# Kernel tuning notes

Hardware: AMD Instinct MI355X
Metric: run time of the kernel (lower is better)

Reference implementation:

```python
import jax, jax.numpy as jnp
import numpy as np

TMSG = 15  # max_len - 1


def setup_inputs() -> dict:
    key = jax.random.key(0)
    ks = jax.random.split(key, 8)
    B, T_in, E, H, V = 4096, 4, 256, 512, 32000
    s = lambda k, shape: jax.random.normal(k, shape, jnp.float32) * 0.05
    return {
        "inp": jax.random.normal(ks[0], (B, T_in, E), jnp.float32),
        "Wx0": s(ks[1], (E, 4 * H)),
        "Wh0": s(ks[2], (H, 4 * H)),
        "b0": jnp.zeros((4 * H,), jnp.float32),
        "Wx1": s(ks[3], (H, 4 * H)),
        "Wh1": s(ks[4], (H, 4 * H)),
        "b1": jnp.zeros((4 * H,), jnp.float32),
        "Wd": s(ks[5], (H, V)),
        "bd": jnp.zeros((V,), jnp.float32),
    }


def _lstm_step(x, h, c, Wx, Wh, b):
    # Keras LSTMCell gate order: i, f, g(cell), o
    z = x @ Wx + h @ Wh + b
    i, f, g, o = jnp.split(z, 4, axis=-1)
    c = jax.nn.sigmoid(f) * c + jax.nn.sigmoid(i) * jnp.tanh(g)
    h = jax.nn.sigmoid(o) * jnp.tanh(c)
    return h, c


def reference(inp, Wx0, Wh0, b0, Wx1, Wh1, b1, Wd, bd):
    B = inp.shape[0]
    H = Wh0.shape[0]
    z = jnp.zeros((B, H), inp.dtype)

    def scan_fn(carry, x_t):
        h0, c0, h1, c1 = carry
        h0, c0 = _lstm_step(x_t, h0, c0, Wx0, Wh0, b0)
        h1, c1 = _lstm_step(h0, h1, c1, Wx1, Wh1, b1)
        return (h0, c0, h1, c1), None

    # NOTE: source bug resets initial_state to None every step, so each of the
    # max_len-1 steps runs the identical stacked LSTM from zero state; we run it once.
    (h0, c0, h1, c1), _ = jax.lax.scan(scan_fn, (z, z, z, z), jnp.swapaxes(inp, 0, 1))
    out = h1  # (B, H) last-step output of top cell

    log_probs = jax.nn.log_softmax(out @ Wd + bd, axis=-1)  # (B, V)
    probs = jnp.exp(log_probs)
    entropy = -jnp.sum(probs * log_probs, axis=-1)  # (B,)

    keys = jax.random.split(jax.random.key(42), TMSG)
    samples = jax.vmap(lambda k: jax.random.categorical(k, log_probs, axis=-1))(keys)  # (T, B)
    lp = log_probs[jnp.arange(B)[None, :], samples]  # (T, B) log_prob of sampled chars
    ent = jnp.broadcast_to(entropy[None], (TMSG, B))  # (T, B)

    message = samples.T  # (B, T)
    message = jnp.concatenate([message, jnp.zeros_like(message)], axis=1)  # (B, 2T)
    state_h = jnp.stack([h0, c0])  # keras unpack quirk: states[0] = [h, c] of cell 0
    return (message, lp, ent, state_h)
```

## Files before the change

### kernel.cpp

```cpp
#include <hip/hip_runtime.h>
#include <stdint.h>
#include <math.h>

#define BB 4096
#define HH 512
#define VV 32000
#define NT 15
#define STF 2097152

struct KeysArg { uint32_t w[2*NT]; };

__host__ __device__ inline void tf2x32(uint32_t k0, uint32_t k1,
                                       uint32_t x0, uint32_t x1,
                                       uint32_t& o0, uint32_t& o1) {
  uint32_t ks2 = k0 ^ k1 ^ 0x1BD11BDAu;
  x0 += k0; x1 += k1;
#define TF_R(r) { x0 += x1; x1 = (x1 << (r)) | (x1 >> (32 - (r))); x1 ^= x0; }
  TF_R(13) TF_R(15) TF_R(26) TF_R(6)
  x0 += k1; x1 += ks2 + 1u;
  TF_R(17) TF_R(29) TF_R(16) TF_R(24)
  x0 += ks2; x1 += k0 + 2u;
  TF_R(13) TF_R(15) TF_R(26) TF_R(6)
  x0 += k0; x1 += k1 + 3u;
  TF_R(17) TF_R(29) TF_R(16) TF_R(24)
  x0 += k1; x1 += ks2 + 4u;
  TF_R(13) TF_R(15) TF_R(26) TF_R(6)
  x0 += ks2; x1 += k0 + 5u;
#undef TF_R
  o0 = x0; o1 = x1;
}

__device__ inline void gll16(const float* g, float* l) {
  __builtin_amdgcn_global_load_lds(
      (const __attribute__((address_space(1))) void*)g,
      (__attribute__((address_space(3))) void*)l, 16, 0, 0);
}

__global__ __launch_bounds__(256)
void gemm_sk(const float* __restrict__ A0, int lda0,
             const float* __restrict__ W0, int koff0, int Klen0,
             const float* __restrict__ A1, int lda1,
             const float* __restrict__ W1, int koff1, int Klen1,
             int ldw,
             const float* __restrict__ bias,
             float* __restrict__ C0, float* __restrict__ C1, int ldc)
{
  const float* A; const float* W; float* C; int lda, koff, Klen;
  if (blockIdx.z == 0) { A = A0; lda = lda0; W = W0; koff = koff0; Klen = Klen0; C = C0; }
  else                 { A = A1; lda = lda1; W = W1; koff = koff1; Klen = Klen1; C = C1; }

  __shared__ float As[2][128 * 16];
  __shared__ float Ws[2][16 * 128];
  const int tid = threadIdx.x;
  const int lane = tid & 63, wv = tid >> 6;
  const int m0 = blockIdx.y * 128;
  const int n0 = blockIdx.x * 128;
  const int tx = tid & 15, ty = tid >> 4;

  float acc[8][8];
  #pragma unroll
  for (int i = 0; i < 8; ++i)
    #pragma unroll
    for (int j = 0; j < 8; ++j) acc[i][j] = 0.0f;

  const int a_row_in = (lane >> 2);
  const int a_chunk  = (lane & 3) * 4;
  const int w_row_in = (lane >> 5);
  const int w_col    = (lane & 31) * 4;

  auto STAGE = [&](int buf, int kt) {
    const int k0 = koff + (kt << 4);
    #pragma unroll
    for (int i = 0; i < 2; ++i) {
      const int seg = wv * 2 + i;
      const int arow = seg * 16 + a_row_in;
      gll16(A + (size_t)(m0 + arow) * lda + (k0 + a_chunk),
            &As[buf][seg * 256]);
      const int wrow = seg * 2 + w_row_in;
      gll16(W + (size_t)(k0 + wrow) * ldw + (n0 + w_col),
            &Ws[buf][seg * 256]);
    }
  };

  const int nkt = Klen >> 4;
  STAGE(0, 0);
  asm volatile("s_waitcnt vmcnt(0)" ::: "memory");
  __syncthreads();

  int cur = 0;
  for (int kt = 0; kt < nkt; ++kt) {
    if (kt + 1 < nkt) STAGE(cur ^ 1, kt + 1);
    #pragma unroll
    for (int kk4 = 0; kk4 < 4; ++kk4) {
      float4 a4[8];
      #pragma unroll
      for (int mm = 0; mm < 8; ++mm)
        a4[mm] = *(const float4*)&As[cur][(ty * 8 + mm) * 16 + kk4 * 4];
      #pragma unroll
      for (int q = 0; q < 4; ++q) {
        const int kk = kk4 * 4 + q;
        float4 b0 = *(const float4*)&Ws[cur][kk * 128 + tx * 4];
        float4 b1 = *(const float4*)&Ws[cur][kk * 128 + tx * 4 + 64];
        float br[8] = {b0.x,b0.y,b0.z,b0.w,b1.x,b1.y,b1.z,b1.w};
        #pragma unroll
        for (int mm = 0; mm < 8; ++mm) {
          float av = (q == 0) ? a4[mm].x : (q == 1) ? a4[mm].y
                   : (q == 2) ? a4[mm].z : a4[mm].w;
          #pragma unroll
          for (int j = 0; j < 8; ++j)
            acc[mm][j] = fmaf(av, br[j], acc[mm][j]);
        }
      }
    }
    asm volatile("s_waitcnt vmcnt(0)" ::: "memory");
    __syncthreads();
    cur ^= 1;
  }

  const int wn = tx * 4;
  #pragma unroll
  for (int i = 0; i < 8; ++i) {
    const int m = m0 + ty * 8 + i;
    float* dst = C + (size_t)m * ldc + (n0 + wn);
    float4 o0, o1;
    o0.x = acc[i][0]; o0.y = acc[i][1]; o0.z = acc[i][2]; o0.w = acc[i][3];
    o1.x = acc[i][4]; o1.y = acc[i][5]; o1.z = acc[i][6]; o1.w = acc[i][7];
    if (bias) {
      o0.x += bias[n0+wn+0]; o0.y += bias[n0+wn+1];
      o0.z += bias[n0+wn+2]; o0.w += bias[n0+wn+3];
      o1.x += bias[n0+wn+64]; o1.y += bias[n0+wn+65];
      o1.z += bias[n0+wn+66]; o1.w += bias[n0+wn+67];
    }
    *(float4*)dst        = o0;
    *(float4*)(dst + 64) = o1;
  }
}

__global__ __launch_bounds__(256)
void gate_kernel(const float* __restrict__ z0, const float* __restrict__ z1,
                 const float* __restrict__ bias,
                 const float* __restrict__ cin,
                 float* __restrict__ hout, float* __restrict__ cout,
                 float* __restrict__ sh, float* __restrict__ sc)
{
  int idx = blockIdx.x * 256 + threadIdx.x;
  int b = idx >> 9, j = idx & 511;
  const size_t r2 = (size_t)b * 2048;
  float zi = z0[r2+j]      + z1[r2+j]      + bias[j];
  float zf = z0[r2+j+512]  + z1[r2+j+512]  + bias[j+512];
  float zg = z0[r2+j+1024] + z1[r2+j+1024] + bias[j+1024];
  float zo = z0[r2+j+1536] + z1[r2+j+1536] + bias[j+1536];
  float si = 1.0f/(1.0f+expf(-zi));
  float sf = 1.0f/(1.0f+expf(-zf));
  float so = 1.0f/(1.0f+expf(-zo));
  float c = sf * cin[idx] + si * tanhf(zg);
  float h = so * tanhf(c);
  cout[idx] = c; hout[idx] = h;
  if (sh) { sh[idx] = h; sc[idx] = c; }
}

__global__ __launch_bounds__(256)
void rowstat_kernel(const float* __restrict__ logits,
                    float* __restrict__ rowM, float* __restrict__ rowLS,
                    float* __restrict__ rowEnt)
{
  const int row = blockIdx.x;
  const float* x = logits + (size_t)row * VV;
  const int tid = threadIdx.x;
  float m = -INFINITY;
  for (int v = tid; v < VV; v += 256) m = fmaxf(m, x[v]);
  #pragma unroll
  for (int off = 32; off; off >>= 1) m = fmaxf(m, __shfl_down(m, off));
  __shared__ float sm[4], ssum[4], swsum[4];
  if ((tid & 63) == 0) sm[tid >> 6] = m;
  __syncthreads();
  m = fmaxf(fmaxf(sm[0], sm[1]), fmaxf(sm[2], sm[3]));
  float s = 0.0f, w = 0.0f;
  for (int v = tid; v < VV; v += 256) {
    float d = x[v] - m;
    float e = expf(d);
    s += e; w += d * e;
  }
  #pragma unroll
  for (int off = 32; off; off >>= 1) { s += __shfl_down(s, off); w += __shfl_down(w, off); }
  if ((tid & 63) == 0) { ssum[tid >> 6] = s; swsum[tid >> 6] = w; }
  __syncthreads();
  if (tid == 0) {
    s = ssum[0]+ssum[1]+ssum[2]+ssum[3];
    w = swsum[0]+swsum[1]+swsum[2]+swsum[3];
    float ls = logf(s);
    rowM[row] = m; rowLS[row] = ls; rowEnt[row] = ls - w / s;
  }
}

__global__ __launch_bounds__(256)
void sample_kernel(const float* __restrict__ logits,
                   const float* __restrict__ rowM, const float* __restrict__ rowLS,
                   const float* __restrict__ rowEnt,
                   float* __restrict__ out,
                   KeysArg keys, int bbase)
{
  const int l = blockIdx.x;
  const int b = bbase + l;
  const float* x = logits + (size_t)l * VV;
  const float m = rowM[l], ls = rowLS[l];

  float bv[NT];
  uint32_t bi[NT];
  float thr[NT];
  #pragma unroll
  for (int t = 0; t < NT; ++t) { bv[t] = -INFINITY; bi[t] = 0; thr[t] = 1.0f; }

  const uint32_t pbase = (uint32_t)b * (uint32_t)VV;
  for (int v = threadIdx.x; v < VV; v += 256) {
    const float lp = (x[v] - m) - ls;
    const uint32_t p = pbase + (uint32_t)v;
    #pragma unroll
    for (int t = 0; t < NT; ++t) {
      uint32_t o0, o1;
      tf2x32(keys.w[2*t], keys.w[2*t+1], 0u, p, o0, o1);
      const uint32_t bits = o0 ^ o1;
      const float uf = __uint_as_float((bits >> 9) | 0x3f800000u);
      if (__any(uf >= thr[t])) {
        float u = fmaxf(uf - 1.0f, 1.17549435e-38f);
        float g = -logf(-logf(u)) + lp;
        bool improved = (uf >= thr[t]) && (g > bv[t]);
        if (improved) { bv[t] = g; bi[t] = (uint32_t)v; }
        if (__any(improved)) {
          float wb = bv[t];
          #pragma unroll
          for (int off = 1; off < 64; off <<= 1)
            wb = fmaxf(wb, __shfl_xor(wb, off));
          float us = expf(-expf(-(wb + ls)));
          thr[t] = 1.0f + us * 0.999999f;
        }
      }
    }
  }

  __shared__ float rv[NT][4];
  __shared__ uint32_t ri[NT][4];
  const int lane = threadIdx.x & 63, wq = threadIdx.x >> 6;
  #pragma unroll
  for (int t = 0; t < NT; ++t) {
    float v = bv[t]; uint32_t idx = bi[t];
    #pragma unroll
    for (int off = 32; off; off >>= 1) {
      float ov = __shfl_down(v, off);
      uint32_t oi = __shfl_down(idx, off);
      if (ov > v || (ov == v && oi < idx)) { v = ov; idx = oi; }
    }
    if (lane == 0) { rv[t][wq] = v; ri[t][wq] = idx; }
  }
  __syncthreads();
  if (threadIdx.x < NT) {
    const int t = threadIdx.x;
    float v = rv[t][0]; uint32_t idx = ri[t][0];
    #pragma unroll
    for (int q = 1; q < 4; ++q) {
      float ov = rv[t][q]; uint32_t oi = ri[t][q];
      if (ov > v || (ov == v && oi < idx)) { v = ov; idx = oi; }
    }
    out[(size_t)b * 30 + t]      = (float)idx;
    out[(size_t)b * 30 + 15 + t] = 0.0f;
    out[122880 + (size_t)t * BB + b] = (x[idx] - m) - ls;
    out[184320 + (size_t)t * BB + b] = rowEnt[l];
  }
}

extern "C" void kernel_launch(void* const* d_in, const int* in_sizes, int n_in,
                              void* d_out, int out_size, void* d_ws, size_t ws_size,
                              hipStream_t stream)
{
  const float* inp = (const float*)d_in[0];
  const float* Wx0 = (const float*)d_in[1];
  const float* Wh0 = (const float*)d_in[2];
  const float* b0v = (const float*)d_in[3];
  const float* Wx1 = (const float*)d_in[4];
  const float* Wh1 = (const float*)d_in[5];
  const float* b1v = (const float*)d_in[6];
  const float* Wd  = (const float*)d_in[7];
  const float* bdv = (const float*)d_in[8];
  float* out = (float*)d_out;
  float* ws = (float*)d_ws;

  float* h0 = ws;
  float* c0 = ws + (size_t)STF;
  float* h1 = ws + (size_t)2*STF;
  float* c1 = ws + (size_t)3*STF;
  float* rowM  = ws + (size_t)4*STF;
  float* rowLS = rowM + 4096;
  float* rowEnt = rowLS + 4096;
  float* region = ws + (size_t)4*STF + 12288;
  float* z0 = region;
  float* z1 = region + (size_t)4096*2048;
  float* logits = region;

  size_t ws_floats = ws_size / 4;
  size_t base = (size_t)4*STF + 12288;
  int CH = 4096;
  while (CH > 128 && base + (size_t)CH*VV > ws_floats) CH >>= 1;

  hipMemsetAsync(ws, 0, (size_t)4*STF*sizeof(float), stream);

  for (int t = 0; t < 4; ++t) {
    gemm_sk<<<dim3(2048/128, 4096/128, 2), 256, 0, stream>>>(
        h0, 512, Wh0, 0, 512,
        inp + t*256, 1024, Wx0, 0, 256,
        2048, nullptr, z0, z1, 2048);
    gate_kernel<<<STF/256, 256, 0, stream>>>(
        z0, z1, b0v, c0, h0, c0,
        (t==3) ? out + 245760 : (float*)nullptr,
        (t==3) ? out + 245760 + STF : (float*)nullptr);
    gemm_sk<<<dim3(2048/128, 4096/128, 2), 256, 0, stream>>>(
        h0, 512, Wx1, 0, 512,
        h1, 512, Wh1, 0, 512,
        2048, nullptr, z0, z1, 2048);
    gate_kernel<<<STF/256, 256, 0, stream>>>(
        z0, z1, b1v, c1, h1, c1, (float*)nullptr, (float*)nullptr);
  }

  KeysArg ka;
  for (int t = 0; t < NT; ++t) {
    uint32_t o0, o1;
    tf2x32(0u, 42u, 0u, (uint32_t)t, o0, o1);
    ka.w[2*t] = o0; ka.w[2*t+1] = o1;
  }

  const int nch = 4096 / CH;
  for (int c = 0; c < nch; ++c) {
    int bbase = c * CH;
    gemm_sk<<<dim3(VV/128, CH/128, 1), 256, 0, stream>>>(
        h1 + (size_t)bbase*512, 512, Wd, 0, 512,
        nullptr, 0, nullptr, 0, 0,
        VV, bdv, logits, nullptr, VV);
    rowstat_kernel<<<CH, 256, 0, stream>>>(logits, rowM, rowLS, rowEnt);
    sample_kernel<<<CH, 256, 0, stream>>>(logits, rowM, rowLS, rowEnt, out, ka, bbase);
  }
}
```

Measured before the change: 7.285 ms.

## Fuse sampling with next-chunk logits GEMM in one launch via double buffering

Measured after the change: 7.216 ms. Within noise of the previous version (-0.9%).

```diff
diff --git a/kernel.cpp b/kernel.cpp
--- a/kernel.cpp
+++ b/kernel.cpp
@@ -7,6 +7,7 @@
 #define VV 32000
 #define NT 15
 #define STF 2097152
+#define NXT 250
 
 struct KeysArg { uint32_t w[2*NT]; };
 
@@ -73,11 +74,9 @@
     #pragma unroll
     for (int i = 0; i < 2; ++i) {
       const int seg = wv * 2 + i;
-      const int arow = seg * 16 + a_row_in;
-      gll16(A + (size_t)(m0 + arow) * lda + (k0 + a_chunk),
+      gll16(A + (size_t)(m0 + seg * 16 + a_row_in) * lda + (k0 + a_chunk),
             &As[buf][seg * 256]);
-      const int wrow = seg * 2 + w_row_in;
-      gll16(W + (size_t)(k0 + wrow) * ldw + (n0 + w_col),
+      gll16(W + (size_t)(k0 + seg * 2 + w_row_in) * ldw + (n0 + w_col),
             &Ws[buf][seg * 256]);
     }
   };
@@ -194,77 +193,162 @@
 }
 
 __global__ __launch_bounds__(256)
-void sample_kernel(const float* __restrict__ logits,
-                   const float* __restrict__ rowM, const float* __restrict__ rowLS,
-                   const float* __restrict__ rowEnt,
-                   float* __restrict__ out,
-                   KeysArg keys, int bbase)
+void fused_sg(const float* __restrict__ logitsS,
+              const float* __restrict__ rowM, const float* __restrict__ rowLS,
+              const float* __restrict__ rowEnt,
+              float* __restrict__ out, KeysArg keys, int bbaseS, int SB,
+              const float* __restrict__ AG, const float* __restrict__ Wd,
+              const float* __restrict__ bd, float* __restrict__ logitsG)
 {
-  const int l = blockIdx.x;
-  const int b = bbase + l;
-  const float* x = logits + (size_t)l * VV;
-  const float m = rowM[l], ls = rowLS[l];
-
-  float bv[NT];
-  uint32_t bi[NT];
-  float thr[NT];
-  #pragma unroll
-  for (int t = 0; t < NT; ++t) { bv[t] = -INFINITY; bi[t] = 0; thr[t] = 1.0f; }
-
-  const uint32_t pbase = (uint32_t)b * (uint32_t)VV;
-  for (int v = threadIdx.x; v < VV; v += 256) {
-    const float lp = (x[v] - m) - ls;
-    const uint32_t p = pbase + (uint32_t)v;
-    #pragma unroll
-    for (int t = 0; t < NT; ++t) {
-      uint32_t o0, o1;
-      tf2x32(keys.w[2*t], keys.w[2*t+1], 0u, p, o0, o1);
-      const uint32_t bits = o0 ^ o1;
-      const float uf = __uint_as_float((bits >> 9) | 0x3f800000u);
-      if (__any(uf >= thr[t])) {
-        float u = fmaxf(uf - 1.0f, 1.17549435e-38f);
-        float g = -logf(-logf(u)) + lp;
-        bool improved = (uf >= thr[t]) && (g > bv[t]);
-        if (improved) { bv[t] = g; bi[t] = (uint32_t)v; }
-        if (__any(improved)) {
-          float wb = bv[t];
-          #pragma unroll
-          for (int off = 1; off < 64; off <<= 1)
-            wb = fmaxf(wb, __shfl_xor(wb, off));
-          float us = expf(-expf(-(wb + ls)));
-          thr[t] = 1.0f + us * 0.999999f;
+  __shared__ float As[2][128 * 16];
+  __shared__ float Ws[2][16 * 128];
+  __shared__ float rv[NT][4];
+  __shared__ uint32_t ri[NT][4];
+
+  const int tid = threadIdx.x;
+
+  if ((int)blockIdx.x < SB) {
+    const int l = blockIdx.x;
+    const int b = bbaseS + l;
+    const float* x = logitsS + (size_t)l * VV;
+    const float m = rowM[l], ls = rowLS[l];
+
+    float bv[NT];
+    uint32_t bi[NT];
+    float thr[NT];
+    #pragma unroll
+    for (int t = 0; t < NT; ++t) { bv[t] = -INFINITY; bi[t] = 0; thr[t] = 1.0f; }
+
+    const uint32_t pbase = (uint32_t)b * (uint32_t)VV;
+    for (int v = tid; v < VV; v += 256) {
+      const float lp = (x[v] - m) - ls;
+      const uint32_t p = pbase + (uint32_t)v;
+      #pragma unroll
+      for (int t = 0; t < NT; ++t) {
+        uint32_t o0, o1;
+        tf2x32(keys.w[2*t], keys.w[2*t+1], 0u, p, o0, o1);
+        const uint32_t bits = o0 ^ o1;
+        const float uf = __uint_as_float((bits >> 9) | 0x3f800000u);
+        if (__any(uf >= thr[t])) {
+          float u = fmaxf(uf - 1.0f, 1.17549435e-38f);
+          float g = -logf(-logf(u)) + lp;
+          bool improved = (uf >= thr[t]) && (g > bv[t]);
+          if (improved) { bv[t] = g; bi[t] = (uint32_t)v; }
+          if (__any(improved)) {
+            float wb = bv[t];
+            #pragma unroll
+            for (int off = 1; off < 64; off <<= 1)
+              wb = fmaxf(wb, __shfl_xor(wb, off));
+            float us = expf(-expf(-(wb + ls)));
+            thr[t] = 1.0f + us * 0.999999f;
+          }
         }
       }
     }
-  }
-
-  __shared__ float rv[NT][4];
-  __shared__ uint32_t ri[NT][4];
-  const int lane = threadIdx.x & 63, wq = threadIdx.x >> 6;
-  #pragma unroll
-  for (int t = 0; t < NT; ++t) {
-    float v = bv[t]; uint32_t idx = bi[t];
-    #pragma unroll
-    for (int off = 32; off; off >>= 1) {
-      float ov = __shfl_down(v, off);
-      uint32_t oi = __shfl_down(idx, off);
-      if (ov > v || (ov == v && oi < idx)) { v = ov; idx = oi; }
-    }
-    if (lane == 0) { rv[t][wq] = v; ri[t][wq] = idx; }
-  }
+
+    const int lane = tid & 63, wq = tid >> 6;
+    #pragma unroll
+    for (int t = 0; t < NT; ++t) {
+      float v = bv[t]; uint32_t idx = bi[t];
+      #pragma unroll
+      for (int off = 32; off; off >>= 1) {
+        float ov = __shfl_down(v, off);
+        uint32_t oi = __shfl_down(idx, off);
+        if (ov > v || (ov == v && oi < idx)) { v = ov; idx = oi; }
+      }
+      if (lane == 0) { rv[t][wq] = v; ri[t][wq] = idx; }
+    }
+    __syncthreads();
+    if (tid < NT) {
+      const int t = tid;
+      float v = rv[t][0]; uint32_t idx = ri[t][0];
+      #pragma unroll
+      for (int q = 1; q < 4; ++q) {
+        float ov = rv[t][q]; uint32_t oi = ri[t][q];
+        if (ov > v || (ov == v && oi < idx)) { v = ov; idx = oi; }
+      }
+      out[(size_t)b * 30 + t]      = (float)idx;
+      out[(size_t)b * 30 + 15 + t] = 0.0f;
+      out[122880 + (size_t)t * BB + b] = (x[idx] - m) - ls;
+      out[184320 + (size_t)t * BB + b] = rowEnt[l];
+    }
+    return;
+  }
+
+  const int gb = (int)blockIdx.x - SB;
+  const int m0 = (gb / NXT) * 128;
+  const int n0 = (gb % NXT) * 128;
+  const int lane = tid & 63, wv = tid >> 6;
+  const int tx = tid & 15, ty = tid >> 4;
+
+  float acc[8][8];
+  #pragma unroll
+  for (int i = 0; i < 8; ++i)
+    #pragma unroll
+    for (int j = 0; j < 8; ++j) acc[i][j] = 0.0f;
+
+  const int a_row_in = (lane >> 2);
+  const int a_chunk  = (lane & 3) * 4;
+  const int w_row_in = (lane >> 5);
+  const int w_col    = (lane & 31) * 4;
+
+  auto STAGE = [&](int buf, int kt) {
+    const int k0 = kt << 4;
+    #pragma unroll
+    for (int i = 0; i < 2; ++i) {
+      const int seg = wv * 2 + i;
+      gll16(AG + (size_t)(m0 + seg * 16 + a_row_in) * 512 + (k0 + a_chunk),
+            &As[buf][seg * 256]);
+      gll16(Wd + (size_t)(k0 + seg * 2 + w_row_in) * VV + (n0 + w_col),
+            &Ws[buf][seg * 256]);
+    }
+  };
+
+  STAGE(0, 0);
+  asm volatile("s_waitcnt vmcnt(0)" ::: "memory");
   __syncthreads();
-  if (threadIdx.x < NT) {
-    const int t = threadIdx.x;
-    float v = rv[t][0]; uint32_t idx = ri[t][0];
-    #pragma unroll
-    for (int q = 1; q < 4; ++q) {
-      float ov = rv[t][q]; uint32_t oi = ri[t][q];
-      if (ov > v || (ov == v && oi < idx)) { v = ov; idx = oi; }
-    }
-    out[(size_t)b * 30 + t]      = (float)idx;
-    out[(size_t)b * 30 + 15 + t] = 0.0f;
-    out[122880 + (size_t)t * BB + b] = (x[idx] - m) - ls;
-    out[184320 + (size_t)t * BB + b] = rowEnt[l];
+
+  int cur = 0;
+  for (int kt = 0; kt < 32; ++kt) {
+    if (kt + 1 < 32) STAGE(cur ^ 1, kt + 1);
+    #pragma unroll
+    for (int kk4 = 0; kk4 < 4; ++kk4) {
+      float4 a4[8];
+      #pragma unroll
+      for (int mm = 0; mm < 8; ++mm)
+        a4[mm] = *(const float4*)&As[cur][(ty * 8 + mm) * 16 + kk4 * 4];
+      #pragma unroll
+      for (int q = 0; q < 4; ++q) {
+        const int kk = kk4 * 4 + q;
+        float4 b0 = *(const float4*)&Ws[cur][kk * 128 + tx * 4];
+        float4 b1 = *(const float4*)&Ws[cur][kk * 128 + tx * 4 + 64];
+        float br[8] = {b0.x,b0.y,b0.z,b0.w,b1.x,b1.y,b1.z,b1.w};
+        #pragma unroll
+        for (int mm = 0; mm < 8; ++mm) {
+          float av = (q == 0) ? a4[mm].x : (q == 1) ? a4[mm].y
+                   : (q == 2) ? a4[mm].z : a4[mm].w;
+          #pragma unroll
+          for (int j = 0; j < 8; ++j)
+            acc[mm][j] = fmaf(av, br[j], acc[mm][j]);
+        }
+      }
+    }
+    asm volatile("s_waitcnt vmcnt(0)" ::: "memory");
+    __syncthreads();
+    cur ^= 1;
+  }
+
+  const int wn = tx * 4;
+  #pragma unroll
+  for (int i = 0; i < 8; ++i) {
+    float* dst = logitsG + (size_t)(m0 + ty * 8 + i) * VV + (n0 + wn);
+    float4 o0, o1;
+    o0.x = acc[i][0] + bd[n0+wn+0];  o0.y = acc[i][1] + bd[n0+wn+1];
+    o0.z = acc[i][2] + bd[n0+wn+2];  o0.w = acc[i][3] + bd[n0+wn+3];
+    o1.x = acc[i][4] + bd[n0+wn+64]; o1.y = acc[i][5] + bd[n0+wn+65];
+    o1.z = acc[i][6] + bd[n0+wn+66]; o1.w = acc[i][7] + bd[n0+wn+67];
+    *(float4*)dst        = o0;
+    *(float4*)(dst + 64) = o1;
   }
 }
 
@@ -288,18 +372,22 @@
   float* c0 = ws + (size_t)STF;
   float* h1 = ws + (size_t)2*STF;
   float* c1 = ws + (size_t)3*STF;
-  float* rowM  = ws + (size_t)4*STF;
-  float* rowLS = rowM + 4096;
-  float* rowEnt = rowLS + 4096;
+  float* rowM0  = ws + (size_t)4*STF;
+  float* rowLS0 = rowM0 + 1024;
+  float* rowEnt0 = rowLS0 + 1024;
+  float* rowM1  = rowEnt0 + 1024;
+  float* rowLS1 = rowM1 + 1024;
+  float* rowEnt1 = rowLS1 + 1024;
   float* region = ws + (size_t)4*STF + 12288;
   float* z0 = region;
   float* z1 = region + (size_t)4096*2048;
-  float* logits = region;
 
   size_t ws_floats = ws_size / 4;
   size_t base = (size_t)4*STF + 12288;
-  int CH = 4096;
-  while (CH > 128 && base + (size_t)CH*VV > ws_floats) CH >>= 1;
+  int CH = 512;
+  while (CH > 128 && base + (size_t)2*CH*VV > ws_floats) CH >>= 1;
+  float* logitsA = region;
+  float* logitsB = region + (size_t)CH*VV;
 
   hipMemsetAsync(ws, 0, (size_t)4*STF*sizeof(float), stream);
 
@@ -328,13 +416,28 @@
   }
 
   const int nch = 4096 / CH;
+  const int GB = NXT * (CH / 128);
+
+  fused_sg<<<GB, 256, 0, stream>>>(
+      nullptr, nullptr, nullptr, nullptr, out, ka, 0, 0,
+      h1, Wd, bdv, logitsA);
+  rowstat_kernel<<<CH, 256, 0, stream>>>(logitsA, rowM0, rowLS0, rowEnt0);
+
   for (int c = 0; c < nch; ++c) {
-    int bbase = c * CH;
-    gemm_sk<<<dim3(VV/128, CH/128, 1), 256, 0, stream>>>(
-        h1 + (size_t)bbase*512, 512, Wd, 0, 512,
-        nullptr, 0, nullptr, 0, 0,
-        VV, bdv, logits, nullptr, VV);
-    rowstat_kernel<<<CH, 256, 0, stream>>>(logits, rowM, rowLS, rowEnt);
-    sample_kernel<<<CH, 256, 0, stream>>>(logits, rowM, rowLS, rowEnt, out, ka, bbase);
-  }
-}
+    float* lgS = (c & 1) ? logitsB : logitsA;
+    float* lgG = (c & 1) ? logitsA : logitsB;
+    float* rM = (c & 1) ? rowM1 : rowM0;
+    float* rL = (c & 1) ? rowLS1 : rowLS0;
+    float* rE = (c & 1) ? rowEnt1 : rowEnt0;
+    const bool more = (c + 1 < nch);
+    fused_sg<<<CH + (more ? GB : 0), 256, 0, stream>>>(
+        lgS, rM, rL, rE, out, ka, c * CH, CH,
+        more ? (h1 + (size_t)(c + 1) * CH * 512) : h1, Wd, bdv, lgG);
+    if (more) {
+      float* rM2 = (c & 1) ? rowM0 : rowM1;
+      float* rL2 = (c & 1) ? rowLS0 : rowLS1;
+      float* rE2 = (c & 1) ? rowEnt0 : rowEnt1;
+      rowstat_kernel<<<CH, 256, 0, stream>>>(lgG, rM2, rL2, rE2);
+    }
+  }
+}
```
